# Optimization experiments

Hardware: AMD Instinct MI355X
Metric: run time of the kernel (lower is better)

Reference implementation:

```python
import jax, jax.numpy as jnp
import numpy as np

B = 256          # graphs per batch
NR = 268         # ROIs (nodes) per graph
N = B * NR       # total nodes
IC, OC = 256, 64 # in/out channels
NC = 7           # communities
DEG = 32
E = N * DEG      # total edges
K = int(NR * 0.8)  # 214 nodes kept per graph (floor, as torch .long())
LN_EPS = 1e-5


def setup_inputs() -> dict:
    key = jax.random.key(0)
    ks = jax.random.split(key, 10)
    x = jax.random.normal(ks[0], (N, IC), jnp.float32)
    # within-graph random edges: local src/dst in [0, NR) plus per-graph offset
    src = jax.random.randint(ks[1], (E,), 0, NR, dtype=jnp.int32)
    dst = jax.random.randint(ks[2], (E,), 0, NR, dtype=jnp.int32)
    off = jnp.repeat(jnp.arange(B, dtype=jnp.int32) * NR, NR * DEG)
    edge_index = jnp.stack([src + off, dst + off])  # (2, E)
    edge_attr = jax.random.uniform(ks[3], (E, 1), jnp.float32)
    batch = jnp.repeat(jnp.arange(B, dtype=jnp.int32), NR)
    xav = lambda k, shp: jax.random.normal(k, shp, jnp.float32) * np.float32(
        np.sqrt(2.0 / (shp[-2] + shp[-1])))
    return {
        "x": x, "edge_index": edge_index, "edge_attr": edge_attr, "batch": batch,
        "basis_kernels": xav(ks[4], (NC, IC, OC)),
        "roi_community": xav(ks[5], (NR, NC)),
        "ew_w": xav(ks[6], (1, OC)), "ew_b": jnp.zeros((OC,), jnp.float32),
        "conv_bias": jnp.zeros((OC,), jnp.float32),
        "ln_gamma": jnp.ones((OC,), jnp.float32), "ln_beta": jnp.zeros((OC,), jnp.float32),
        "att_w1": xav(ks[7], (OC, OC)), "att_b1": jnp.zeros((OC,), jnp.float32),
        "att_w2": xav(ks[8], (OC, 1)), "att_b2": jnp.zeros((1,), jnp.float32),
    }


def reference(x, edge_index, edge_attr, batch, basis_kernels, roi_community,
              ew_w, ew_b, conv_bias, ln_gamma, ln_beta,
              att_w1, att_b1, att_w2, att_b2):
    n = x.shape[0]
    loops = jnp.arange(n, dtype=edge_index.dtype)
    ei = jnp.concatenate([edge_index, jnp.stack([loops, loops])], axis=1)  # add self loops
    ea = jnp.concatenate([edge_attr, jnp.ones((n, 1), x.dtype)], axis=0)   # fill_value=1.0

    # ROI-aware kernels: per-node mixture of basis kernels
    cw = jax.nn.softmax(roi_community, axis=-1)            # (NR, NC)
    roi_k = jnp.einsum('rc,cio->rio', cw, basis_kernels)   # (NR, IC, OC)
    node_ids = loops % NR
    node_k = roi_k[node_ids]                               # (N, IC, OC) gather
    xt = jnp.einsum('ni,nio->no', x, node_k)               # per-node bmm

    # edge-gated message passing, scatter-add aggregation
    gate = jax.nn.sigmoid(ea @ ew_w + ew_b)                # (E+N, OC)
    msg = xt[ei[0]] * gate
    out = jax.ops.segment_sum(msg, ei[1], num_segments=n) + conv_bias

    out = jax.nn.elu(out)
    mu = jnp.mean(out, axis=-1, keepdims=True)
    var = jnp.mean(jnp.square(out - mu), axis=-1, keepdims=True)
    h = (out - mu) * jax.lax.rsqrt(var + LN_EPS) * ln_gamma + ln_beta
    # dropout: eval mode (identity)

    # R-pool: per-graph top-k (all graphs have NR contiguous nodes)
    scores = (jnp.tanh(h @ att_w1 + att_b1) @ att_w2 + att_b2).squeeze(-1)  # (N,)
    top_v, top_i = jax.lax.top_k(scores.reshape(B, NR), K)                  # (B, K)
    perm = (top_i.astype(jnp.int32) + jnp.arange(B, dtype=jnp.int32)[:, None] * NR).reshape(-1)
    x_pooled = h[perm] * jax.nn.sigmoid(top_v.reshape(-1))[:, None]
    batch_pooled = batch[perm]
    return x_pooled, batch_pooled, scores, perm
```

## Files before the change

kernel.cpp:

```cpp
#include <hip/hip_runtime.h>
#include <cstdint>
#include <cstddef>

#define NR   268
#define NB   256
#define NN   (NR*NB)
#define IC   256
#define OC   64
#define DEG  32
#define EPG  (NR*DEG)
#define NE   (NN*DEG)
#define KK   214

#define XP_OFF 0
#define BP_OFF 3506176
#define SC_OFF 3560960
#define PM_OFF 3629568

#define WS_ROIK 0
#define WS_XT   4390912
#define WS_HB   8781824
#define WS_META 13172736
#define WS_ROWS 17563648

__global__ __launch_bounds__(256) void k_roik(const float* __restrict__ rc,
                                              const float* __restrict__ basis,
                                              float* __restrict__ roik) {
    int r = blockIdx.x;
    float c[7];
    float m = -1e30f;
#pragma unroll
    for (int j = 0; j < 7; ++j) { c[j] = rc[r*7 + j]; m = fmaxf(m, c[j]); }
    float s = 0.f;
#pragma unroll
    for (int j = 0; j < 7; ++j) { c[j] = expf(c[j] - m); s += c[j]; }
    float inv = 1.f / s;
#pragma unroll
    for (int j = 0; j < 7; ++j) c[j] *= inv;
    for (int idx = threadIdx.x; idx < IC*OC; idx += 256) {
        float acc = 0.f;
#pragma unroll
        for (int j = 0; j < 7; ++j) acc = fmaf(c[j], basis[j*IC*OC + idx], acc);
        roik[(size_t)r*IC*OC + idx] = acc;
    }
}

#define GS3 132
__global__ __launch_bounds__(512) void k_xtf(const float* __restrict__ x,
                                             const float* __restrict__ roik,
                                             float* __restrict__ xt) {
    __shared__ float sXT[32 * GS3];

    int bid = blockIdx.x;
    int r = bid % NR;
    int half = bid / NR;
    int tid = threadIdx.x;
    int lane = tid & 63;
    int wu = __builtin_amdgcn_readfirstlane(tid >> 6);
    int g0 = lane * 2;
    int o0 = wu * 8;

    const float* __restrict__ wk = roik + (size_t)r * (IC*OC);

    int sg = tid & 127, kseg = (tid >> 7) * 8;
    const float* __restrict__ xrow =
        x + ((size_t)(half*128 + sg) * NR + r) * IC + kseg;

    float acc[2][8];
#pragma unroll
    for (int i = 0; i < 2; ++i)
#pragma unroll
        for (int j = 0; j < 8; ++j) acc[i][j] = 0.f;

    for (int kt = 0; kt < IC; kt += 32) {
        __syncthreads();
#pragma unroll
        for (int u = 0; u < 8; u += 4) {
            float4 xv = *(const float4*)(xrow + kt + u);
            sXT[(kseg+u+0)*GS3 + sg] = xv.x;
            sXT[(kseg+u+1)*GS3 + sg] = xv.y;
            sXT[(kseg+u+2)*GS3 + sg] = xv.z;
            sXT[(kseg+u+3)*GS3 + sg] = xv.w;
        }
        __syncthreads();

#pragma unroll 8
        for (int k = 0; k < 32; ++k) {
            float2 xa = *(const float2*)&sXT[k*GS3 + g0];
            const float* wrow = wk + (size_t)(kt + k) * OC + o0;
#pragma unroll
            for (int j = 0; j < 8; ++j) {
                float wv = wrow[j];
                acc[0][j] = fmaf(xa.x, wv, acc[0][j]);
                acc[1][j] = fmaf(xa.y, wv, acc[1][j]);
            }
        }
    }

#pragma unroll
    for (int i = 0; i < 2; ++i) {
        int g = half*128 + g0 + i;
        float* p = xt + ((size_t)g * NR + r) * OC + o0;
        float4 a; a.x = acc[i][0]; a.y = acc[i][1]; a.z = acc[i][2]; a.w = acc[i][3];
        float4 b; b.x = acc[i][4]; b.y = acc[i][5]; b.z = acc[i][6]; b.w = acc[i][7];
        *(float4*)p = a;
        *(float4*)(p + 4) = b;
    }
}

#define NREP2 16
__global__ __launch_bounds__(1024) void k_csr(const int* __restrict__ ei,
                                              const float* __restrict__ ea,
                                              float2* __restrict__ meta,
                                              unsigned int* __restrict__ rows) {
    int g = blockIdx.x;
    __shared__ unsigned int cnt[NREP2][NR];
    __shared__ unsigned int cur[NREP2][NR];
    __shared__ unsigned int tot[NR];
    __shared__ unsigned int rs[NR];
    int tid = threadIdx.x;
    int wid = tid >> 6;
    for (int i = tid; i < NREP2*NR; i += 1024) ((unsigned*)cnt)[i] = 0u;
    __syncthreads();
    int ebase = g * EPG;
    for (int e = tid; e < EPG; e += 1024) {
        int ld = ei[NE + ebase + e] - g * NR;
        atomicAdd(&cnt[wid][ld], 1u);
    }
    __syncthreads();
    for (int r = tid; r < NR; r += 1024) {
        unsigned t = 0;
#pragma unroll
        for (int s = 0; s < NREP2; ++s) t += cnt[s][r];
        tot[r] = t;
    }
    __syncthreads();
    if (tid < 64) {
        unsigned run = 0;
        for (int base = 0; base < NR; base += 64) {
            int idx = base + tid;
            unsigned v = (idx < NR) ? tot[idx] : 0u;
            unsigned orig = v;
#pragma unroll
            for (int s = 1; s < 64; s <<= 1) {
                int t = __shfl_up((int)v, (unsigned)s, 64);
                if (tid >= s) v += (unsigned)t;
            }
            if (idx < NR) rs[idx] = run + v - orig;
            run += (unsigned)__shfl((int)v, 63, 64);
        }
    }
    __syncthreads();
    for (int r = tid; r < NR; r += 1024) {
        unsigned base = rs[r];
#pragma unroll
        for (int s = 0; s < NREP2; ++s) { cur[s][r] = base; base += cnt[s][r]; }
    }
    __syncthreads();
    for (int i = tid; i < NR + 1; i += 1024)
        rows[(size_t)g * (NR + 1) + i] = (i < NR) ? rs[i] : (unsigned)EPG;
    for (int e = tid; e < EPG; e += 1024) {
        int src = ei[ebase + e];
        int dst = ei[NE + ebase + e];
        float a = ea[ebase + e];
        int ld = dst - g * NR;
        unsigned pos = atomicAdd(&cur[wid][ld], 1u);
        float2 mv; mv.x = __int_as_float((src - g*NR) * OC); mv.y = a;
        meta[(size_t)ebase + pos] = mv;
    }
}

__global__ __launch_bounds__(1024, 4) void k_fused(
    const float* __restrict__ xt,
    const float2* __restrict__ meta,
    const unsigned int* __restrict__ rows,
    float* __restrict__ hbw,
    const float* __restrict__ ew_w, const float* __restrict__ ew_b,
    const float* __restrict__ conv_bias,
    const float* __restrict__ ln_g, const float* __restrict__ ln_b,
    const float* __restrict__ w1, const float* __restrict__ b1,
    const float* __restrict__ w2, const float* __restrict__ b2,
    float* __restrict__ out)
{
    extern __shared__ float xts[];
    __shared__ float rowbuf[16][OC];
    __shared__ float scl[NR];
    __shared__ unsigned long long keys[512];

    int g = blockIdx.x;
    int tid = threadIdx.x;
    int o = tid & 63, w = tid >> 6;

    {
        const float4* s4 = (const float4*)(xt + (size_t)g * NR * OC);
        float4* d4 = (float4*)xts;
        for (int i = tid; i < NR*OC/4; i += 1024) d4[i] = s4[i];
    }

    float wo = ew_w[o], bo = ew_b[o], cb = conv_bias[o];
    float lng = ln_g[o], lnb = ln_b[o];
    float w2o = w2[o], b1o = b1[o], b2s = b2[0];
    float sgself = 1.f / (1.f + expf(-(wo + bo)));

    float z0 = fmaf(0.5f, wo, bo);
    float s  = 1.f / (1.f + expf(-z0));
    float u  = s * (1.f - s);
    float d2 = u * (1.f - 2.f*s);
    float d3 = u * (1.f - 6.f*u);
    float d4c = d2 * (1.f - 12.f*u);
    float k1 = u * wo;
    float k2 = d2 * wo*wo * 0.5f;
    float k3 = d3 * wo*wo*wo * (1.f/6.f);
    float k4 = d4c * wo*wo*wo*wo * (1.f/24.f);
    #define GATE(a_) fmaf(fmaf(fmaf(fmaf(k4,(a_),k3),(a_),k2),(a_),k1),(a_),s)

    #define LOADW(j) float4 wc##j = make_float4(w1[(4*j+0)*OC+o], w1[(4*j+1)*OC+o], \
                                                w1[(4*j+2)*OC+o], w1[(4*j+3)*OC+o]);
    LOADW(0)  LOADW(1)  LOADW(2)  LOADW(3)
    LOADW(4)  LOADW(5)  LOADW(6)  LOADW(7)
    LOADW(8)  LOADW(9)  LOADW(10) LOADW(11)
    LOADW(12) LOADW(13) LOADW(14) LOADW(15)
    #undef LOADW

    const float2* __restrict__ gm = meta + (size_t)g * EPG;
    const unsigned int* __restrict__ gr = rows + (size_t)g * (NR + 1);
    __syncthreads();

    for (int r = w; r < NR; r += 16) {
        unsigned js = gr[r], je = gr[r + 1];
        float acc = xts[r*OC + o] * sgself;
        unsigned j = js;
        for (; j + 8 <= je; j += 8) {
            float2 m0 = gm[j],   m1 = gm[j+1], m2 = gm[j+2], m3 = gm[j+3];
            float2 m4 = gm[j+4], m5 = gm[j+5], m6 = gm[j+6], m7 = gm[j+7];
            float x0 = xts[__float_as_int(m0.x) + o];
            float x1 = xts[__float_as_int(m1.x) + o];
            float x2 = xts[__float_as_int(m2.x) + o];
            float x3 = xts[__float_as_int(m3.x) + o];
            float x4 = xts[__float_as_int(m4.x) + o];
            float x5 = xts[__float_as_int(m5.x) + o];
            float x6 = xts[__float_as_int(m6.x) + o];
            float x7 = xts[__float_as_int(m7.x) + o];
            acc = fmaf(x0, GATE(m0.y - 0.5f), acc);
            acc = fmaf(x1, GATE(m1.y - 0.5f), acc);
            acc = fmaf(x2, GATE(m2.y - 0.5f), acc);
            acc = fmaf(x3, GATE(m3.y - 0.5f), acc);
            acc = fmaf(x4, GATE(m4.y - 0.5f), acc);
            acc = fmaf(x5, GATE(m5.y - 0.5f), acc);
            acc = fmaf(x6, GATE(m6.y - 0.5f), acc);
            acc = fmaf(x7, GATE(m7.y - 0.5f), acc);
        }
        for (; j < je; ++j) {
            float2 m = gm[j];
            float xv = xts[__float_as_int(m.x) + o];
            acc = fmaf(xv, GATE(m.y - 0.5f), acc);
        }
        acc += cb;
        float v = acc > 0.f ? acc : expm1f(acc);
        float s1 = v;
#pragma unroll
        for (int m = 1; m < 64; m <<= 1) s1 += __shfl_xor(s1, m, 64);
        float mu = s1 * (1.f/64.f);
        float d = v - mu;
        float s2 = d * d;
#pragma unroll
        for (int m = 1; m < 64; m <<= 1) s2 += __shfl_xor(s2, m, 64);
        float rsd = rsqrtf(s2 * (1.f/64.f) + 1e-5f);
        float h = fmaf(d * rsd, lng, lnb);
        hbw[((size_t)g * NR + r)*OC + o] = h;
        rowbuf[w][o] = h;
        {
            const float* hr = rowbuf[w];
            float t0 = b1o, t1 = 0.f, t2 = 0.f, t3 = 0.f;
            #define STEP(j) { float4 h4 = *(const float4*)(hr + 4*j); \
                t0 = fmaf(h4.x, wc##j.x, t0); t1 = fmaf(h4.y, wc##j.y, t1); \
                t2 = fmaf(h4.z, wc##j.z, t2); t3 = fmaf(h4.w, wc##j.w, t3); }
            STEP(0)  STEP(1)  STEP(2)  STEP(3)
            STEP(4)  STEP(5)  STEP(6)  STEP(7)
            STEP(8)  STEP(9)  STEP(10) STEP(11)
            STEP(12) STEP(13) STEP(14) STEP(15)
            #undef STEP
            float t = (t0 + t1) + (t2 + t3);
            float a2 = fminf(fmaxf(2.f * t, -80.f), 80.f);
            float y = expf(a2);
            float th = (y - 1.f) / (y + 1.f);
            float p = th * w2o;
#pragma unroll
            for (int m = 1; m < 64; m <<= 1) p += __shfl_xor(p, m, 64);
            if (o == 0) {
                float sc = p + b2s;
                scl[r] = sc;
                out[SC_OFF + (size_t)g * NR + r] = sc;
            }
        }
    }
    #undef GATE
    __syncthreads();

    for (int i = tid; i < 512; i += 1024) {
        unsigned long long key = 0ull;
        if (i < NR) {
            unsigned ub = __float_as_uint(scl[i]);
            unsigned ou = (ub & 0x80000000u) ? ~ub : (ub | 0x80000000u);
            key = (((unsigned long long)ou) << 32) |
                  (unsigned long long)(0xFFFFFFFFu - (unsigned)i);
        }
        keys[i] = key;
    }
    for (int kk = 2; kk <= 512; kk <<= 1) {
        for (int j = kk >> 1; j > 0; j >>= 1) {
            __syncthreads();
            if (tid < 256) {
                int i = ((tid & ~(j - 1)) << 1) | (tid & (j - 1));
                int p = i | j;
                unsigned long long a = keys[i], bb = keys[p];
                bool desc = ((i & kk) == 0);
                if (desc ? (a < bb) : (a > bb)) { keys[i] = bb; keys[p] = a; }
            }
        }
    }
    __syncthreads();

    for (int k = w; k < KK; k += 16) {
        unsigned long long kv = keys[k];
        int r = (int)(0xFFFFFFFFu - (unsigned)(kv & 0xFFFFFFFFull));
        float v = scl[r];
        float gate = 1.f / (1.f + expf(-v));
        float hvv = hbw[((size_t)g * NR + r)*OC + o];
        out[XP_OFF + ((size_t)g*KK + k)*64 + o] = hvv * gate;
        if (o == 0) {
            out[BP_OFF + (size_t)g*KK + k] = (float)g;
            out[PM_OFF + (size_t)g*KK + k] = (float)(g*NR + r);
        }
    }
}

extern "C" void kernel_launch(void* const* d_in, const int* in_sizes, int n_in,
                              void* d_out, int out_size, void* d_ws, size_t ws_size,
                              hipStream_t stream) {
    const float* x     = (const float*)d_in[0];
    const int*   ei    = (const int*)d_in[1];
    const float* ea    = (const float*)d_in[2];
    const float* basis = (const float*)d_in[4];
    const float* rc    = (const float*)d_in[5];
    const float* ew_w  = (const float*)d_in[6];
    const float* ew_b  = (const float*)d_in[7];
    const float* cbias = (const float*)d_in[8];
    const float* ln_g  = (const float*)d_in[9];
    const float* ln_b  = (const float*)d_in[10];
    const float* w1    = (const float*)d_in[11];
    const float* b1    = (const float*)d_in[12];
    const float* w2    = (const float*)d_in[13];
    const float* b2    = (const float*)d_in[14];
    float* out = (float*)d_out;

    float* wsf = (float*)d_ws;
    float* roik = wsf + WS_ROIK;
    float* xtb  = wsf + WS_XT;
    float* hbw  = wsf + WS_HB;
    float2* meta = (float2*)(wsf + WS_META);
    unsigned int* rows = (unsigned int*)(wsf + WS_ROWS);

    k_roik <<<dim3(NR),   dim3(256), 0, stream>>>(rc, basis, roik);
    k_xtf  <<<dim3(NR*2), dim3(512), 0, stream>>>(x, roik, xtb);
    k_csr  <<<dim3(NB),   dim3(1024), 0, stream>>>(ei, ea, meta, rows);
    k_fused<<<dim3(NB),   dim3(1024), NR*OC*sizeof(float), stream>>>(
                                                  xtb, meta, rows, hbw,
                                                  ew_w, ew_b, cbias, ln_g, ln_b,
                                                  w1, b1, w2, b2, out);
}
```

Before: 340.0 us.

## Pack edges into pairs for packed FMA and keep LN output in LDS

The CSR build now groups each row's edges into pairs and stores them as float4 records (two source offsets, two pre-shifted attributes). Odd-length rows are padded with a zero row in LDS. The aggregation loop and the attention MLP now use v_pk_fma_f32 to evaluate two gate polynomials and two products per instruction. The layer-normed features stay in LDS instead of going through a global workspace buffer, which removes a global write and read. The cost is double LDS usage per block, which can lower occupancy, plus extra padding work.

```diff
diff --git a/kernel.cpp b/kernel.cpp
--- a/kernel.cpp
+++ b/kernel.cpp
@@ -19,9 +19,19 @@
 
 #define WS_ROIK 0
 #define WS_XT   4390912
-#define WS_HB   8781824
-#define WS_META 13172736
-#define WS_ROWS 17563648
+#define WS_META 8781824
+#define WS_ROWS 13369344
+
+#define PPG   4480
+#define ZROW  (NR*OC)
+
+typedef float v2f __attribute__((ext_vector_type(2)));
+
+__device__ __forceinline__ v2f pkfma(v2f a, v2f b, v2f c) {
+    v2f d;
+    asm("v_pk_fma_f32 %0, %1, %2, %3" : "=v"(d) : "v"(a), "v"(b), "v"(c));
+    return d;
+}
 
 __global__ __launch_bounds__(256) void k_roik(const float* __restrict__ rc,
                                               const float* __restrict__ basis,
@@ -111,13 +121,13 @@
 #define NREP2 16
 __global__ __launch_bounds__(1024) void k_csr(const int* __restrict__ ei,
                                               const float* __restrict__ ea,
-                                              float2* __restrict__ meta,
+                                              float* __restrict__ meta,
                                               unsigned int* __restrict__ rows) {
     int g = blockIdx.x;
     __shared__ unsigned int cnt[NREP2][NR];
     __shared__ unsigned int cur[NREP2][NR];
     __shared__ unsigned int tot[NR];
-    __shared__ unsigned int rs[NR];
+    __shared__ unsigned int prs[NR];
     int tid = threadIdx.x;
     int wid = tid >> 6;
     for (int i = tid; i < NREP2*NR; i += 1024) ((unsigned*)cnt)[i] = 0u;
@@ -139,42 +149,52 @@
         unsigned run = 0;
         for (int base = 0; base < NR; base += 64) {
             int idx = base + tid;
-            unsigned v = (idx < NR) ? tot[idx] : 0u;
+            unsigned v = (idx < NR) ? ((tot[idx] + 1u) >> 1) : 0u;
             unsigned orig = v;
 #pragma unroll
             for (int s = 1; s < 64; s <<= 1) {
                 int t = __shfl_up((int)v, (unsigned)s, 64);
                 if (tid >= s) v += (unsigned)t;
             }
-            if (idx < NR) rs[idx] = run + v - orig;
+            if (idx < NR) prs[idx] = run + v - orig;
             run += (unsigned)__shfl((int)v, 63, 64);
         }
     }
     __syncthreads();
     for (int r = tid; r < NR; r += 1024) {
-        unsigned base = rs[r];
+        unsigned base = 0;
 #pragma unroll
         for (int s = 0; s < NREP2; ++s) { cur[s][r] = base; base += cnt[s][r]; }
     }
     __syncthreads();
+    unsigned lastPairs = (tot[NR-1] + 1u) >> 1;
     for (int i = tid; i < NR + 1; i += 1024)
-        rows[(size_t)g * (NR + 1) + i] = (i < NR) ? rs[i] : (unsigned)EPG;
+        rows[(size_t)g * (NR + 1) + i] =
+            (i < NR) ? prs[i] : (prs[NR-1] + lastPairs);
+    float* mg = meta + (size_t)g * PPG * 4;
     for (int e = tid; e < EPG; e += 1024) {
         int src = ei[ebase + e];
-        int dst = ei[NE + ebase + e];
+        int ld  = ei[NE + ebase + e] - g * NR;
         float a = ea[ebase + e];
-        int ld = dst - g * NR;
-        unsigned pos = atomicAdd(&cur[wid][ld], 1u);
-        float2 mv; mv.x = __int_as_float((src - g*NR) * OC); mv.y = a;
-        meta[(size_t)ebase + pos] = mv;
+        unsigned rank = atomicAdd(&cur[wid][ld], 1u);
+        unsigned p = prs[ld] + (rank >> 1), sl = rank & 1u;
+        mg[(size_t)p*4 + sl]     = __int_as_float((src - g*NR) * OC);
+        mg[(size_t)p*4 + 2 + sl] = a - 0.5f;
+    }
+    __syncthreads();
+    for (int r = tid; r < NR; r += 1024) {
+        if (tot[r] & 1u) {
+            unsigned p = prs[r] + (tot[r] >> 1);
+            mg[(size_t)p*4 + 1] = __int_as_float(ZROW);
+            mg[(size_t)p*4 + 3] = 0.f;
+        }
     }
 }
 
 __global__ __launch_bounds__(1024, 4) void k_fused(
     const float* __restrict__ xt,
-    const float2* __restrict__ meta,
+    const float4* __restrict__ meta,
     const unsigned int* __restrict__ rows,
-    float* __restrict__ hbw,
     const float* __restrict__ ew_w, const float* __restrict__ ew_b,
     const float* __restrict__ conv_bias,
     const float* __restrict__ ln_g, const float* __restrict__ ln_b,
@@ -182,7 +202,9 @@
     const float* __restrict__ w2, const float* __restrict__ b2,
     float* __restrict__ out)
 {
-    extern __shared__ float xts[];
+    extern __shared__ float smem[];
+    float* xts = smem;
+    float* hls = smem + (NR*OC + 64);
     __shared__ float rowbuf[16][OC];
     __shared__ float scl[NR];
     __shared__ unsigned long long keys[512];
@@ -195,6 +217,7 @@
         const float4* s4 = (const float4*)(xt + (size_t)g * NR * OC);
         float4* d4 = (float4*)xts;
         for (int i = tid; i < NR*OC/4; i += 1024) d4[i] = s4[i];
+        if (tid < 16) d4[NR*OC/4 + tid] = make_float4(0.f, 0.f, 0.f, 0.f);
     }
 
     float wo = ew_w[o], bo = ew_b[o], cb = conv_bias[o];
@@ -203,60 +226,57 @@
     float sgself = 1.f / (1.f + expf(-(wo + bo)));
 
     float z0 = fmaf(0.5f, wo, bo);
-    float s  = 1.f / (1.f + expf(-z0));
-    float u  = s * (1.f - s);
-    float d2 = u * (1.f - 2.f*s);
+    float sg0 = 1.f / (1.f + expf(-z0));
+    float u  = sg0 * (1.f - sg0);
+    float d2 = u * (1.f - 2.f*sg0);
     float d3 = u * (1.f - 6.f*u);
     float d4c = d2 * (1.f - 12.f*u);
     float k1 = u * wo;
     float k2 = d2 * wo*wo * 0.5f;
     float k3 = d3 * wo*wo*wo * (1.f/6.f);
     float k4 = d4c * wo*wo*wo*wo * (1.f/24.f);
-    #define GATE(a_) fmaf(fmaf(fmaf(fmaf(k4,(a_),k3),(a_),k2),(a_),k1),(a_),s)
-
-    #define LOADW(j) float4 wc##j = make_float4(w1[(4*j+0)*OC+o], w1[(4*j+1)*OC+o], \
-                                                w1[(4*j+2)*OC+o], w1[(4*j+3)*OC+o]);
+    v2f kd4 = {k4, k4}, kd3 = {k3, k3}, kd2 = {k2, k2}, kd1 = {k1, k1};
+    v2f sdv = {sg0, sg0};
+
+    #define LOADW(j) \
+        v2f wcA##j = { w1[(4*j+0)*OC+o], w1[(4*j+1)*OC+o] }; \
+        v2f wcB##j = { w1[(4*j+2)*OC+o], w1[(4*j+3)*OC+o] };
     LOADW(0)  LOADW(1)  LOADW(2)  LOADW(3)
     LOADW(4)  LOADW(5)  LOADW(6)  LOADW(7)
     LOADW(8)  LOADW(9)  LOADW(10) LOADW(11)
     LOADW(12) LOADW(13) LOADW(14) LOADW(15)
     #undef LOADW
 
-    const float2* __restrict__ gm = meta + (size_t)g * EPG;
+    const float4* __restrict__ gm = meta + (size_t)g * PPG;
     const unsigned int* __restrict__ gr = rows + (size_t)g * (NR + 1);
-    __syncthreads();
+    const float* __restrict__ xo = xts + o;
+    __syncthreads();
+
+    #define PAIR(mp, acc) { \
+        v2f xv; \
+        xv.x = xo[__float_as_int((mp).x)]; \
+        xv.y = xo[__float_as_int((mp).y)]; \
+        v2f dv = { (mp).z, (mp).w }; \
+        v2f t = pkfma(kd4, dv, kd3); \
+        t = pkfma(t, dv, kd2); \
+        t = pkfma(t, dv, kd1); \
+        t = pkfma(t, dv, sdv); \
+        acc = pkfma(xv, t, acc); }
 
     for (int r = w; r < NR; r += 16) {
         unsigned js = gr[r], je = gr[r + 1];
-        float acc = xts[r*OC + o] * sgself;
+        v2f acc; acc.x = xts[r*OC + o] * sgself; acc.y = 0.f;
         unsigned j = js;
-        for (; j + 8 <= je; j += 8) {
-            float2 m0 = gm[j],   m1 = gm[j+1], m2 = gm[j+2], m3 = gm[j+3];
-            float2 m4 = gm[j+4], m5 = gm[j+5], m6 = gm[j+6], m7 = gm[j+7];
-            float x0 = xts[__float_as_int(m0.x) + o];
-            float x1 = xts[__float_as_int(m1.x) + o];
-            float x2 = xts[__float_as_int(m2.x) + o];
-            float x3 = xts[__float_as_int(m3.x) + o];
-            float x4 = xts[__float_as_int(m4.x) + o];
-            float x5 = xts[__float_as_int(m5.x) + o];
-            float x6 = xts[__float_as_int(m6.x) + o];
-            float x7 = xts[__float_as_int(m7.x) + o];
-            acc = fmaf(x0, GATE(m0.y - 0.5f), acc);
-            acc = fmaf(x1, GATE(m1.y - 0.5f), acc);
-            acc = fmaf(x2, GATE(m2.y - 0.5f), acc);
-            acc = fmaf(x3, GATE(m3.y - 0.5f), acc);
-            acc = fmaf(x4, GATE(m4.y - 0.5f), acc);
-            acc = fmaf(x5, GATE(m5.y - 0.5f), acc);
-            acc = fmaf(x6, GATE(m6.y - 0.5f), acc);
-            acc = fmaf(x7, GATE(m7.y - 0.5f), acc);
+        for (; j + 4 <= je; j += 4) {
+            float4 m0 = gm[j], m1 = gm[j+1], m2 = gm[j+2], m3 = gm[j+3];
+            PAIR(m0, acc) PAIR(m1, acc) PAIR(m2, acc) PAIR(m3, acc)
         }
         for (; j < je; ++j) {
-            float2 m = gm[j];
-            float xv = xts[__float_as_int(m.x) + o];
-            acc = fmaf(xv, GATE(m.y - 0.5f), acc);
-        }
-        acc += cb;
-        float v = acc > 0.f ? acc : expm1f(acc);
+            float4 m0 = gm[j];
+            PAIR(m0, acc)
+        }
+        float accs = acc.x + acc.y + cb;
+        float v = accs > 0.f ? accs : expm1f(accs);
         float s1 = v;
 #pragma unroll
         for (int m = 1; m < 64; m <<= 1) s1 += __shfl_xor(s1, m, 64);
@@ -267,20 +287,20 @@
         for (int m = 1; m < 64; m <<= 1) s2 += __shfl_xor(s2, m, 64);
         float rsd = rsqrtf(s2 * (1.f/64.f) + 1e-5f);
         float h = fmaf(d * rsd, lng, lnb);
-        hbw[((size_t)g * NR + r)*OC + o] = h;
+        hls[r*OC + o] = h;
         rowbuf[w][o] = h;
         {
             const float* hr = rowbuf[w];
-            float t0 = b1o, t1 = 0.f, t2 = 0.f, t3 = 0.f;
+            v2f tA = { b1o, 0.f }, tB = { 0.f, 0.f };
             #define STEP(j) { float4 h4 = *(const float4*)(hr + 4*j); \
-                t0 = fmaf(h4.x, wc##j.x, t0); t1 = fmaf(h4.y, wc##j.y, t1); \
-                t2 = fmaf(h4.z, wc##j.z, t2); t3 = fmaf(h4.w, wc##j.w, t3); }
+                v2f hl = { h4.x, h4.y }, hh = { h4.z, h4.w }; \
+                tA = pkfma(hl, wcA##j, tA); tB = pkfma(hh, wcB##j, tB); }
             STEP(0)  STEP(1)  STEP(2)  STEP(3)
             STEP(4)  STEP(5)  STEP(6)  STEP(7)
             STEP(8)  STEP(9)  STEP(10) STEP(11)
             STEP(12) STEP(13) STEP(14) STEP(15)
             #undef STEP
-            float t = (t0 + t1) + (t2 + t3);
+            float t = (tA.x + tA.y) + (tB.x + tB.y);
             float a2 = fminf(fmaxf(2.f * t, -80.f), 80.f);
             float y = expf(a2);
             float th = (y - 1.f) / (y + 1.f);
@@ -294,7 +314,7 @@
             }
         }
     }
-    #undef GATE
+    #undef PAIR
     __syncthreads();
 
     for (int i = tid; i < 512; i += 1024) {
@@ -326,7 +346,7 @@
         int r = (int)(0xFFFFFFFFu - (unsigned)(kv & 0xFFFFFFFFull));
         float v = scl[r];
         float gate = 1.f / (1.f + expf(-v));
-        float hvv = hbw[((size_t)g * NR + r)*OC + o];
+        float hvv = hls[r*OC + o];
         out[XP_OFF + ((size_t)g*KK + k)*64 + o] = hvv * gate;
         if (o == 0) {
             out[BP_OFF + (size_t)g*KK + k] = (float)g;
@@ -357,15 +377,16 @@
     float* wsf = (float*)d_ws;
     float* roik = wsf + WS_ROIK;
     float* xtb  = wsf + WS_XT;
-    float* hbw  = wsf + WS_HB;
-    float2* meta = (float2*)(wsf + WS_META);
+    float* metaF = wsf + WS_META;
     unsigned int* rows = (unsigned int*)(wsf + WS_ROWS);
+
+    size_t fused_lds = (size_t)(NR*OC + 64 + NR*OC) * sizeof(float);
 
     k_roik <<<dim3(NR),   dim3(256), 0, stream>>>(rc, basis, roik);
     k_xtf  <<<dim3(NR*2), dim3(512), 0, stream>>>(x, roik, xtb);
-    k_csr  <<<dim3(NB),   dim3(1024), 0, stream>>>(ei, ea, meta, rows);
-    k_fused<<<dim3(NB),   dim3(1024), NR*OC*sizeof(float), stream>>>(
-                                                  xtb, meta, rows, hbw,
+    k_csr  <<<dim3(NB),   dim3(1024), 0, stream>>>(ei, ea, metaF, rows);
+    k_fused<<<dim3(NB),   dim3(1024), fused_lds, stream>>>(
+                                                  xtb, (const float4*)metaF, rows,
                                                   ew_w, ew_b, cbias, ln_g, ln_b,
                                                   w1, b1, w2, b2, out);
 }
```

Measured after the change: 320.3 us. -5.8%, faster.
